# Performance work log

Measured on AMD Instinct MI355X. Metric: run time of the kernel, lower is better.

The kernel has to match this reference:

```python
import jax, jax.numpy as jnp
import numpy as np

NUM_CLASSES = 4
SMOOTH = 1e-05
W_DICE, W_CE, W_BOUND = 1.0, 1.0, 0.01
BIG = 1e8  # effectively-infinite squared distance


def _edt_sq_pass(f, axis):
    # Exact 1D squared-distance transform along `axis` via min-plus:
    # out[i] = min_j f[j] + (i-j)^2  (brute-force O(n^2), fully vectorized)
    n = f.shape[axis]
    i = jnp.arange(n, dtype=f.dtype)
    d2 = (i[:, None] - i[None, :]) ** 2  # [n, n]
    fm = jnp.moveaxis(f, axis, -1)
    out = jnp.min(fm[..., None, :] + d2, axis=-1)
    return jnp.moveaxis(out, -1, axis)


def _edt(zero_mask):
    # Euclidean distance to the nearest True voxel of zero_mask
    # (equivalent to scipy distance_transform_edt(~zero_mask)'s convention:
    #  distance to nearest zero of the input == nearest True of zero_mask).
    f = jnp.where(zero_mask, 0.0, BIG).astype(jnp.float32)
    for ax in range(f.ndim):
        f = _edt_sq_pass(f, ax)
    return jnp.sqrt(f)


def _signed_distance(mask):
    # mask: bool [D,H,W]; signed distance map: + outside, - inside.
    d_out = _edt(mask)            # distance(1 - mask)
    d_in = _edt(~mask)            # distance(mask)
    sdf = d_out - d_in
    total = jnp.sum(mask)
    size = mask.size
    sdf = jnp.where(total == 0, jnp.ones_like(sdf), sdf)
    sdf = jnp.where(total == size, -jnp.ones_like(sdf), sdf)
    return sdf


def setup_inputs() -> dict:
    key = jax.random.key(0)
    k1, k2 = jax.random.split(key)
    preds = jax.random.normal(k1, (4, NUM_CLASSES, 64, 64, 64), dtype=jnp.float32)
    targets = jax.random.randint(k2, (4, 64, 64, 64), 0, NUM_CLASSES, dtype=jnp.int32)
    return {"preds": preds, "targets": targets}


def reference(preds, targets):
    B = preds.shape[0]
    probs = jax.nn.softmax(preds, axis=1)  # [B,C,D,H,W]

    # --- Soft Dice ---
    onehot = jax.nn.one_hot(targets, NUM_CLASSES, dtype=preds.dtype)  # [B,D,H,W,C]
    onehot = jnp.moveaxis(onehot, -1, 1)  # [B,C,D,H,W]
    inter = jnp.sum(probs * onehot, axis=(2, 3, 4))
    union = jnp.sum(probs, axis=(2, 3, 4)) + jnp.sum(onehot, axis=(2, 3, 4))
    dice = (2.0 * inter + SMOOTH) / (union + SMOOTH)
    l_dice = 1.0 - jnp.mean(dice)

    # --- Cross entropy (mean over all voxels) ---
    logp = jax.nn.log_softmax(preds, axis=1)
    picked = jnp.take_along_axis(logp, targets[:, None].astype(jnp.int32), axis=1)
    l_ce = -jnp.mean(picked)

    # --- Boundary loss (classes 1..C-1) ---
    l_bound = jnp.float32(0.0)
    for c in range(1, NUM_CLASSES):
        mask_c = targets == c  # [B,D,H,W]
        sdf_c = jax.vmap(_signed_distance)(mask_c)  # [B,D,H,W]
        l_bound = l_bound + jnp.sum(jnp.mean(sdf_c * probs[:, c], axis=(1, 2, 3)))
    l_bound = l_bound / (B * (NUM_CLASSES - 1))

    return W_DICE * l_dice + W_CE * l_ce + W_BOUND * l_bound
```

## Files before the change

kernel.cpp:

```cpp
#include <hip/hip_runtime.h>
#include <math.h>

#define NVOX 262144
#define GRID_B 768

__device__ __forceinline__ unsigned short dist2_u16(unsigned long long mask, int w) {
    if (mask == 0ull) return 0xFFFFu;
    unsigned long long mr = mask >> w;
    unsigned long long ml = mask << (63 - w);
    int dr = mr ? __builtin_ctzll(mr) : 127;
    int dl = ml ? __builtin_clzll(ml) : 127;
    int dd = dr < dl ? dr : dl;
    return (unsigned short)(dd * dd);
}

__global__ __launch_bounds__(256) void kB_edt12(
    const int* __restrict__ targets, unsigned short* __restrict__ bufA) {
    __shared__ unsigned short tO[64 * 66];
    __shared__ unsigned short tI[64 * 66];
    int blk = blockIdx.x;
    int cm = blk % 3;
    int bd = blk / 3;
    int d = bd & 63, b = bd >> 6;
    int c = cm + 1;
    int t = threadIdx.x, lane = t & 63, wid = t >> 6;
    const int* tg = targets + (size_t)b * NVOX + (size_t)d * 4096;

    #pragma unroll
    for (int i = 0; i < 16; ++i) {
        int e = t + 256 * i;
        int h = wid + 4 * i;
        int tv = tg[e];
        unsigned long long mask = __ballot(tv == c);
        tO[h * 66 + lane] = dist2_u16(mask, lane);
        tI[h * 66 + lane] = dist2_u16(~mask, lane);
    }
    __syncthreads();

    for (int r = 0; r < 16; ++r) {
        int w = wid * 16 + r;
        {
            unsigned best = tO[lane * 66 + w];
            for (int dk = 1; dk < 64; ++dk) {
                unsigned d2 = (unsigned)(dk * dk);
                if (__all(d2 >= best)) break;
                int hl = lane - dk; hl = hl < 0 ? 0 : hl;
                int hr = lane + dk; hr = hr > 63 ? 63 : hr;
                unsigned ca = tO[hl * 66 + w] + d2;
                unsigned cb = tO[hr * 66 + w] + d2;
                ca = ca < cb ? ca : cb;
                best = best < ca ? best : ca;
            }
            tO[lane * 66 + w] = (unsigned short)best;
        }
        {
            unsigned best = tI[lane * 66 + w];
            for (int dk = 1; dk < 64; ++dk) {
                unsigned d2 = (unsigned)(dk * dk);
                if (__all(d2 >= best)) break;
                int hl = lane - dk; hl = hl < 0 ? 0 : hl;
                int hr = lane + dk; hr = hr > 63 ? 63 : hr;
                unsigned ca = tI[hl * 66 + w] + d2;
                unsigned cb = tI[hr * 66 + w] + d2;
                ca = ca < cb ? ca : cb;
                best = best < ca ? best : ca;
            }
            tI[lane * 66 + w] = (unsigned short)best;
        }
    }
    __syncthreads();

    int combo = b * 3 + cm;
    size_t oO = (size_t)combo * NVOX + (size_t)d * 64;
    size_t oI = (size_t)(combo + 12) * NVOX + (size_t)d * 64;
    #pragma unroll
    for (int i = 0; i < 16; ++i) {
        int h = wid + 4 * i;
        bufA[oO + (size_t)h * 4096 + lane] = tO[h * 66 + lane];
        bufA[oI + (size_t)h * 4096 + lane] = tI[h * 66 + lane];
    }
}

__global__ __launch_bounds__(512) void K2_big(
    const float* __restrict__ preds, const int* __restrict__ targets,
    unsigned short* __restrict__ bufA,
    float* __restrict__ part_stats, float* __restrict__ part_bound) {
    __shared__ unsigned short tile[6][64 * 66];
    __shared__ float sred[8][16];
    __shared__ float bsum[8][3];
    int blk = blockIdx.x;
    int b = blk >> 6, h = blk & 63;
    int t = threadIdx.x, lane = t & 63, wid = t >> 6;

    int e0 = 8 * t, d0 = e0 >> 6, w0 = e0 & 63;
    #pragma unroll
    for (int p = 0; p < 6; ++p) {
        int cm = p >> 1, v = p & 1;
        const unsigned short* src =
            bufA + (size_t)(b * 3 + cm + 12 * v) * NVOX + (size_t)h * 4096 + e0;
        uint4 u = *(const uint4*)src;
        unsigned* dst32 = (unsigned*)&tile[p][d0 * 66 + w0];
        dst32[0] = u.x; dst32[1] = u.y; dst32[2] = u.z; dst32[3] = u.w;
    }

    size_t vbase = (size_t)d0 * 4096 + (size_t)h * 64 + w0;
    const float* pp = preds + (size_t)(b * 4) * NVOX + vbase;
    float4 f[4][2];
    #pragma unroll
    for (int c = 0; c < 4; ++c) {
        f[c][0] = *(const float4*)(pp + (size_t)c * NVOX);
        f[c][1] = *(const float4*)(pp + (size_t)c * NVOX + 4);
    }
    const int* tp = targets + (size_t)b * NVOX + vbase;
    int4 tg0 = *(const int4*)(tp);
    int4 tg1 = *(const int4*)(tp + 4);

    const float L2E = 1.4426950408889634f;
    const float LN2 = 0.6931471805599453f;
    float q[13];
    #pragma unroll
    for (int k = 0; k < 13; ++k) q[k] = 0.0f;
    float pr[3][8];

    #pragma unroll
    for (int j = 0; j < 8; ++j) {
        float a0 = (&f[0][j >> 2].x)[j & 3];
        float a1 = (&f[1][j >> 2].x)[j & 3];
        float a2 = (&f[2][j >> 2].x)[j & 3];
        float a3 = (&f[3][j >> 2].x)[j & 3];
        int tv = (j < 4) ? (&tg0.x)[j] : (&tg1.x)[j - 4];
        float m  = fmaxf(fmaxf(a0, a1), fmaxf(a2, a3));
        float e0_ = exp2f((a0 - m) * L2E);
        float e1_ = exp2f((a1 - m) * L2E);
        float e2_ = exp2f((a2 - m) * L2E);
        float e3_ = exp2f((a3 - m) * L2E);
        float ssum = e0_ + e1_ + e2_ + e3_;
        float inv  = __builtin_amdgcn_rcpf(ssum);
        float p0 = e0_ * inv, p1 = e1_ * inv, p2 = e2_ * inv, p3 = e3_ * inv;
        float xt = (tv == 0) ? a0 : (tv == 1) ? a1 : (tv == 2) ? a2 : a3;
        q[12] += (m - xt) + log2f(ssum) * LN2;
        q[4] += p0; q[5] += p1; q[6] += p2; q[7] += p3;
        if (tv == 0)      { q[0] += p0; q[8]  += 1.0f; }
        else if (tv == 1) { q[1] += p1; q[9]  += 1.0f; }
        else if (tv == 2) { q[2] += p2; q[10] += 1.0f; }
        else              { q[3] += p3; q[11] += 1.0f; }
        pr[0][j] = p1; pr[1][j] = p2; pr[2][j] = p3;
    }
    __syncthreads();

    for (int job = wid; job < 384; job += 8) {
        int p = job >> 6, w = job & 63;
        unsigned short* T = tile[p];
        unsigned best = T[lane * 66 + w];
        for (int dk = 1; dk < 64; ++dk) {
            unsigned d2 = (unsigned)(dk * dk);
            if (__all(d2 >= best)) break;
            int dl = lane - dk; dl = dl < 0 ? 0 : dl;
            int dr = lane + dk; dr = dr > 63 ? 63 : dr;
            unsigned ca = T[dl * 66 + w] + d2;
            unsigned cb = T[dr * 66 + w] + d2;
            ca = ca < cb ? ca : cb;
            best = best < ca ? best : ca;
        }
        T[lane * 66 + w] = (unsigned short)best;
    }
    __syncthreads();

    float accb[3] = {0.0f, 0.0f, 0.0f};
    #pragma unroll
    for (int j = 0; j < 8; ++j) {
        int idx = d0 * 66 + w0 + j;
        #pragma unroll
        for (int cm = 0; cm < 3; ++cm) {
            float dO = (float)tile[2 * cm][idx];
            float dI = (float)tile[2 * cm + 1][idx];
            float sdf = sqrtf(dO) - sqrtf(dI);
            accb[cm] += sdf * pr[cm][j];
        }
    }

    #pragma unroll
    for (int k = 0; k < 13; ++k) {
        float x = q[k];
        #pragma unroll
        for (int o = 32; o > 0; o >>= 1) x += __shfl_down(x, o);
        if (lane == 0) sred[wid][k] = x;
    }
    #pragma unroll
    for (int cm = 0; cm < 3; ++cm) {
        float x = accb[cm];
        #pragma unroll
        for (int o = 32; o > 0; o >>= 1) x += __shfl_down(x, o);
        if (lane == 0) bsum[wid][cm] = x;
    }
    __syncthreads();
    if (t < 13) {
        float s = 0.0f;
        #pragma unroll
        for (int ww = 0; ww < 8; ++ww) s += sred[ww][t];
        part_stats[t * 256 + blk] = s;
    }
    if (t >= 64 && t < 67) {
        int cm = t - 64;
        float s = 0.0f;
        #pragma unroll
        for (int ww = 0; ww < 8; ++ww) s += bsum[ww][cm];
        part_bound[(b * 3 + cm) * 64 + h] = s;
    }
}

__global__ __launch_bounds__(1024) void K3_final(
    const float* __restrict__ part_stats, const float* __restrict__ part_bound,
    float* __restrict__ out) {
    __shared__ float sred[52];
    __shared__ float bred[12];
    __shared__ double S[52];
    int t = threadIdx.x, lane = t & 63, wid = t >> 6;

    if (wid < 4) {
        float v[13];
        #pragma unroll
        for (int k = 0; k < 13; ++k) v[k] = part_stats[k * 256 + t];
        #pragma unroll
        for (int k = 0; k < 13; ++k) {
            float x = v[k];
            #pragma unroll
            for (int o = 32; o > 0; o >>= 1) x += __shfl_down(x, o);
            if (lane == 0) sred[k * 4 + wid] = x;
        }
    } else {
        float bv = part_bound[(wid - 4) * 64 + lane];
        #pragma unroll
        for (int o = 32; o > 0; o >>= 1) bv += __shfl_down(bv, o);
        if (lane == 0) bred[wid - 4] = bv;
    }
    __syncthreads();
    if (t < 52) S[t] = (double)sred[t];
    __syncthreads();
    if (t == 0) {
        const double NV = (double)NVOX;
        double dice_sum = 0.0;
        for (int b = 0; b < 4; ++b)
            for (int c = 0; c < 4; ++c) {
                double inter = S[c * 4 + b];
                double un    = S[(4 + c) * 4 + b] + S[(8 + c) * 4 + b];
                dice_sum += (2.0 * inter + 1e-5) / (un + 1e-5);
            }
        double l_dice = 1.0 - dice_sum / 16.0;
        double l_ce = (S[48] + S[49] + S[50] + S[51]) / (4.0 * NV);
        double lb = 0.0;
        for (int cb = 0; cb < 12; ++cb) {
            int b = cb / 3, c = cb % 3 + 1;
            double cnt = S[(8 + c) * 4 + b];
            double s;
            if (cnt == 0.0)      s =  S[(4 + c) * 4 + b];
            else if (cnt == NV)  s = -S[(4 + c) * 4 + b];
            else                 s =  (double)bred[cb];
            lb += s / NV;
        }
        lb /= 12.0;
        out[0] = (float)(l_dice + l_ce + 0.01 * lb);
    }
}

extern "C" void kernel_launch(void* const* d_in, const int* in_sizes, int n_in,
                              void* d_out, int out_size, void* d_ws, size_t ws_size,
                              hipStream_t stream) {
    const float* preds   = (const float*)d_in[0];
    const int*   targets = (const int*)d_in[1];
    float* out = (float*)d_out;

    unsigned short* bufA = (unsigned short*)d_ws;
    float* part_stats = (float*)(bufA + (size_t)24 * NVOX);
    float* part_bound = part_stats + 13 * 256;

    kB_edt12<<<GRID_B, 256, 0, stream>>>(targets, bufA);
    K2_big<<<256, 512, 0, stream>>>(preds, targets, bufA, part_stats, part_bound);
    K3_final<<<1, 1024, 0, stream>>>(part_stats, part_bound, out);
}
```

Measured before the change: 54.02 us.

## Split K2 blocks along W halves to double grid size, use nontemporal loads

Each K2 block now covers one half of the W dimension for a given (b,h) slice, so the grid doubles from 256 to 512 blocks and each thread handles 4 voxels instead of 8. The D-axis EDT pass only needs the columns in that half, so the shared tile shrinks to 32+2 columns. This is meant to fill more of the machine's compute units and cut per-block latency. The final kernel is reworked to reduce the 512 partials and the 128-per-combo boundary partials. Preds are now read with nontemporal loads.

```diff
diff --git a/kernel.cpp b/kernel.cpp
--- a/kernel.cpp
+++ b/kernel.cpp
@@ -3,6 +3,8 @@
 
 #define NVOX 262144
 #define GRID_B 768
+
+typedef float f32x4 __attribute__((ext_vector_type(4)));
 
 __device__ __forceinline__ unsigned short dist2_u16(unsigned long long mask, int w) {
     if (mask == 0ull) return 0xFFFFu;
@@ -85,50 +87,46 @@
     const float* __restrict__ preds, const int* __restrict__ targets,
     unsigned short* __restrict__ bufA,
     float* __restrict__ part_stats, float* __restrict__ part_bound) {
-    __shared__ unsigned short tile[6][64 * 66];
+    __shared__ unsigned short tile[6][64 * 34];
     __shared__ float sred[8][16];
     __shared__ float bsum[8][3];
     int blk = blockIdx.x;
-    int b = blk >> 6, h = blk & 63;
+    int b = blk >> 7, rem = blk & 127;
+    int h = rem >> 1, wh = rem & 1;
     int t = threadIdx.x, lane = t & 63, wid = t >> 6;
 
-    int e0 = 8 * t, d0 = e0 >> 6, w0 = e0 & 63;
+    int e = 4 * t;
+    int d0 = e >> 5, w0 = e & 31;
+
+    size_t vbase = (size_t)d0 * 4096 + (size_t)h * 64 + wh * 32 + w0;
+    const float* pp = preds + (size_t)(b * 4) * NVOX + vbase;
+    f32x4 f0 = __builtin_nontemporal_load((const f32x4*)(pp));
+    f32x4 f1 = __builtin_nontemporal_load((const f32x4*)(pp + NVOX));
+    f32x4 f2 = __builtin_nontemporal_load((const f32x4*)(pp + 2 * NVOX));
+    f32x4 f3 = __builtin_nontemporal_load((const f32x4*)(pp + 3 * NVOX));
+    int4 tg4 = *(const int4*)(targets + (size_t)b * NVOX + vbase);
+
+    size_t poffg = (size_t)h * 4096 + (size_t)d0 * 64 + wh * 32 + w0;
     #pragma unroll
     for (int p = 0; p < 6; ++p) {
         int cm = p >> 1, v = p & 1;
-        const unsigned short* src =
-            bufA + (size_t)(b * 3 + cm + 12 * v) * NVOX + (size_t)h * 4096 + e0;
-        uint4 u = *(const uint4*)src;
-        unsigned* dst32 = (unsigned*)&tile[p][d0 * 66 + w0];
-        dst32[0] = u.x; dst32[1] = u.y; dst32[2] = u.z; dst32[3] = u.w;
-    }
-
-    size_t vbase = (size_t)d0 * 4096 + (size_t)h * 64 + w0;
-    const float* pp = preds + (size_t)(b * 4) * NVOX + vbase;
-    float4 f[4][2];
-    #pragma unroll
-    for (int c = 0; c < 4; ++c) {
-        f[c][0] = *(const float4*)(pp + (size_t)c * NVOX);
-        f[c][1] = *(const float4*)(pp + (size_t)c * NVOX + 4);
-    }
-    const int* tp = targets + (size_t)b * NVOX + vbase;
-    int4 tg0 = *(const int4*)(tp);
-    int4 tg1 = *(const int4*)(tp + 4);
+        const unsigned short* src = bufA + (size_t)(b * 3 + cm + 12 * v) * NVOX + poffg;
+        uint2 u = *(const uint2*)src;
+        unsigned* dst32 = (unsigned*)&tile[p][d0 * 34 + w0];
+        dst32[0] = u.x; dst32[1] = u.y;
+    }
 
     const float L2E = 1.4426950408889634f;
     const float LN2 = 0.6931471805599453f;
     float q[13];
     #pragma unroll
     for (int k = 0; k < 13; ++k) q[k] = 0.0f;
-    float pr[3][8];
-
-    #pragma unroll
-    for (int j = 0; j < 8; ++j) {
-        float a0 = (&f[0][j >> 2].x)[j & 3];
-        float a1 = (&f[1][j >> 2].x)[j & 3];
-        float a2 = (&f[2][j >> 2].x)[j & 3];
-        float a3 = (&f[3][j >> 2].x)[j & 3];
-        int tv = (j < 4) ? (&tg0.x)[j] : (&tg1.x)[j - 4];
+    float pr[3][4];
+
+    #pragma unroll
+    for (int j = 0; j < 4; ++j) {
+        float a0 = f0[j], a1 = f1[j], a2 = f2[j], a3 = f3[j];
+        int tv = (&tg4.x)[j];
         float m  = fmaxf(fmaxf(a0, a1), fmaxf(a2, a3));
         float e0_ = exp2f((a0 - m) * L2E);
         float e1_ = exp2f((a1 - m) * L2E);
@@ -148,28 +146,28 @@
     }
     __syncthreads();
 
-    for (int job = wid; job < 384; job += 8) {
-        int p = job >> 6, w = job & 63;
+    for (int job = wid; job < 192; job += 8) {
+        int p = job >> 5, w = job & 31;
         unsigned short* T = tile[p];
-        unsigned best = T[lane * 66 + w];
+        unsigned best = T[lane * 34 + w];
         for (int dk = 1; dk < 64; ++dk) {
             unsigned d2 = (unsigned)(dk * dk);
             if (__all(d2 >= best)) break;
             int dl = lane - dk; dl = dl < 0 ? 0 : dl;
             int dr = lane + dk; dr = dr > 63 ? 63 : dr;
-            unsigned ca = T[dl * 66 + w] + d2;
-            unsigned cb = T[dr * 66 + w] + d2;
+            unsigned ca = T[dl * 34 + w] + d2;
+            unsigned cb = T[dr * 34 + w] + d2;
             ca = ca < cb ? ca : cb;
             best = best < ca ? best : ca;
         }
-        T[lane * 66 + w] = (unsigned short)best;
+        T[lane * 34 + w] = (unsigned short)best;
     }
     __syncthreads();
 
     float accb[3] = {0.0f, 0.0f, 0.0f};
     #pragma unroll
-    for (int j = 0; j < 8; ++j) {
-        int idx = d0 * 66 + w0 + j;
+    for (int j = 0; j < 4; ++j) {
+        int idx = d0 * 34 + w0 + j;
         #pragma unroll
         for (int cm = 0; cm < 3; ++cm) {
             float dO = (float)tile[2 * cm][idx];
@@ -198,44 +196,55 @@
         float s = 0.0f;
         #pragma unroll
         for (int ww = 0; ww < 8; ++ww) s += sred[ww][t];
-        part_stats[t * 256 + blk] = s;
+        part_stats[t * 512 + blk] = s;
     }
     if (t >= 64 && t < 67) {
         int cm = t - 64;
         float s = 0.0f;
         #pragma unroll
         for (int ww = 0; ww < 8; ++ww) s += bsum[ww][cm];
-        part_bound[(b * 3 + cm) * 64 + h] = s;
+        part_bound[(b * 3 + cm) * 128 + rem] = s;
     }
 }
 
 __global__ __launch_bounds__(1024) void K3_final(
     const float* __restrict__ part_stats, const float* __restrict__ part_bound,
     float* __restrict__ out) {
-    __shared__ float sred[52];
+    __shared__ float sredf[13 * 8];
     __shared__ float bred[12];
     __shared__ double S[52];
     int t = threadIdx.x, lane = t & 63, wid = t >> 6;
 
-    if (wid < 4) {
+    if (t < 512) {
         float v[13];
         #pragma unroll
-        for (int k = 0; k < 13; ++k) v[k] = part_stats[k * 256 + t];
+        for (int k = 0; k < 13; ++k) v[k] = part_stats[k * 512 + t];
         #pragma unroll
         for (int k = 0; k < 13; ++k) {
             float x = v[k];
             #pragma unroll
             for (int o = 32; o > 0; o >>= 1) x += __shfl_down(x, o);
-            if (lane == 0) sred[k * 4 + wid] = x;
+            if (lane == 0) sredf[k * 8 + wid] = x;
         }
     } else {
-        float bv = part_bound[(wid - 4) * 64 + lane];
+        int m = wid - 8;
+        float bv = part_bound[m * 128 + lane] + part_bound[m * 128 + 64 + lane];
         #pragma unroll
         for (int o = 32; o > 0; o >>= 1) bv += __shfl_down(bv, o);
-        if (lane == 0) bred[wid - 4] = bv;
-    }
-    __syncthreads();
-    if (t < 52) S[t] = (double)sred[t];
+        if (lane == 0) bred[m] = bv;
+        if (m < 4) {
+            int m2 = 8 + m;
+            float b2 = part_bound[m2 * 128 + lane] + part_bound[m2 * 128 + 64 + lane];
+            #pragma unroll
+            for (int o = 32; o > 0; o >>= 1) b2 += __shfl_down(b2, o);
+            if (lane == 0) bred[m2] = b2;
+        }
+    }
+    __syncthreads();
+    if (t < 52) {
+        int k = t >> 2, b = t & 3;
+        S[k * 4 + b] = (double)sredf[k * 8 + 2 * b] + (double)sredf[k * 8 + 2 * b + 1];
+    }
     __syncthreads();
     if (t == 0) {
         const double NV = (double)NVOX;
@@ -272,9 +281,9 @@
 
     unsigned short* bufA = (unsigned short*)d_ws;
     float* part_stats = (float*)(bufA + (size_t)24 * NVOX);
-    float* part_bound = part_stats + 13 * 256;
+    float* part_bound = part_stats + 13 * 512;
 
     kB_edt12<<<GRID_B, 256, 0, stream>>>(targets, bufA);
-    K2_big<<<256, 512, 0, stream>>>(preds, targets, bufA, part_stats, part_bound);
+    K2_big<<<512, 512, 0, stream>>>(preds, targets, bufA, part_stats, part_bound);
     K3_final<<<1, 1024, 0, stream>>>(part_stats, part_bound, out);
 }
```

Measured after the change: 53.93 us. About the same (-0.2%).
